# Kernel tuning notes

Measured on AMD Instinct MI355X. Metric: run time of the kernel, lower is better.

## Reference

```python
import jax, jax.numpy as jnp
import numpy as np

KH = KW = 3
K = KH * KW
STRIDE = 1
PAD = 1
DIL = 1
DG = 1  # deformable groups


def conv2d(x, w, b):
    out = jax.lax.conv_general_dilated(
        x, w, window_strides=(STRIDE, STRIDE),
        padding=[(PAD, PAD), (PAD, PAD)], rhs_dilation=(DIL, DIL),
        dimension_numbers=('NCHW', 'OIHW', 'NCHW'))
    return out + b[None, :, None, None]


def deform_conv2d(x, offset, mask, w, b):
    """DCNv2: bilinear sample at predicted offsets, modulate by mask, GEMM with w."""
    B, Cin, H, W = x.shape
    Ho, Wo = offset.shape[2], offset.shape[3]
    cpg = Cin // DG
    # torchvision layout: channel 2*(g*K+k) = dy, 2*(g*K+k)+1 = dx
    off = offset.reshape(B, DG, K, 2, Ho, Wo)
    off_y, off_x = off[:, :, :, 0], off[:, :, :, 1]  # [B,DG,K,Ho,Wo]
    m = mask.reshape(B, DG, K, Ho, Wo)
    ky = jnp.repeat(jnp.arange(KH), KW) * DIL          # [K] kernel row offsets
    kx = jnp.tile(jnp.arange(KW), KH) * DIL            # [K] kernel col offsets
    hh = jnp.arange(Ho) * STRIDE - PAD
    ww = jnp.arange(Wo) * STRIDE - PAD
    py = off_y + ky[None, None, :, None, None] + hh[None, None, None, :, None]
    px = off_x + kx[None, None, :, None, None] + ww[None, None, None, None, :]
    y0 = jnp.floor(py); x0 = jnp.floor(px)
    wy = py - y0; wx = px - x0
    x_g = x.reshape(B, DG, cpg, H * W)

    def gather(yc, xc):  # zero-padded bilinear corner fetch
        valid = ((yc >= 0) & (yc < H) & (xc >= 0) & (xc < W)).astype(x.dtype)
        yi = jnp.clip(yc, 0, H - 1).astype(jnp.int32)
        xi = jnp.clip(xc, 0, W - 1).astype(jnp.int32)
        idx = (yi * W + xi).reshape(B, DG, 1, K * Ho * Wo)
        v = jnp.take_along_axis(x_g, jnp.broadcast_to(idx, (B, DG, cpg, K * Ho * Wo)), axis=3)
        return v.reshape(B, DG, cpg, K, Ho, Wo) * valid[:, :, None]

    v00 = gather(y0, x0)
    v01 = gather(y0, x0 + 1)
    v10 = gather(y0 + 1, x0)
    v11 = gather(y0 + 1, x0 + 1)
    wy_b = wy[:, :, None]; wx_b = wx[:, :, None]  # broadcast over cpg
    sampled = (v00 * (1 - wy_b) * (1 - wx_b) + v01 * (1 - wy_b) * wx_b
               + v10 * wy_b * (1 - wx_b) + v11 * wy_b * wx_b)
    sampled = (sampled * m[:, :, None]).reshape(B, Cin, K, Ho, Wo)
    Cout = w.shape[0]
    out = jnp.einsum('bckhw,ock->bohw', sampled, w.reshape(Cout, Cin, K))
    return out + b[None, :, None, None]


def setup_inputs() -> dict:
    key = jax.random.key(0)
    k1, k2, k3, k4 = jax.random.split(key, 4)
    B, Cin, Cout, H, W = 8, 128, 128, 64, 64
    omc = DG * 3 * K  # 2*K offsets + K mask channels = 27
    x = jax.random.normal(k1, (B, Cin, H, W), dtype=jnp.float32)
    # small offset-conv weights -> modest predicted offsets (mimics near-zero init)
    w_off = jax.random.normal(k2, (omc, Cin, KH, KW), dtype=jnp.float32) * 0.01
    b_off = jnp.zeros((omc,), dtype=jnp.float32)
    w_def = jax.random.normal(k3, (Cout, Cin, KH, KW), dtype=jnp.float32) * (1.0 / np.sqrt(Cin * K))
    b_def = jax.random.normal(k4, (Cout,), dtype=jnp.float32) * 0.01
    return {"x": x, "w_off": w_off, "b_off": b_off, "w_def": w_def, "b_def": b_def}


def reference(x, w_off, b_off, w_def, b_def):
    out = conv2d(x, w_off, b_off)
    oc = DG * 2 * K
    offset = out[:, :oc]
    mask = jax.nn.sigmoid(out[:, oc:])
    return deform_conv2d(x, offset, mask, w_def, b_def)
```

## Files before the change

kernel.cpp:

```cpp
#include <hip/hip_runtime.h>
#include <math.h>

typedef _Float16 f16;
typedef __attribute__((ext_vector_type(2))) _Float16 f16x2;
typedef __attribute__((ext_vector_type(8))) _Float16 f16x8;
typedef __attribute__((ext_vector_type(4))) float f32x4;

#define NBATCH 8
#define WSA_ELE 36864
#define WSB_ELE 147456
#define OFF_WSB  73728
#define OFF_XT   368640
#define OFF_OFFM 8757248

__device__ __forceinline__ void gload_lds16(const f16* gsrc, f16* ldst) {
  __builtin_amdgcn_global_load_lds(
      (const __attribute__((address_space(1))) unsigned int*)gsrc,
      (__attribute__((address_space(3))) unsigned int*)ldst, 16, 0, 0);
}

__global__ __launch_bounds__(256) void prep_w_kernel(const float* __restrict__ w_off,
                                                     const float* __restrict__ w_def,
                                                     f16* __restrict__ wsA,
                                                     f16* __restrict__ wsB) {
  int i = blockIdx.x * 256 + threadIdx.x;
  if (i < WSA_ELE) {
    int j = i & 7, lane = (i >> 3) & 63, fm = i >> 9;
    int ch = fm >> 1, mt = fm & 1;
    int row = mt * 16 + (lane & 15);
    int kidx = ch * 32 + (lane >> 4) * 8 + j;
    int k = kidx >> 7, cc = kidx & 127;
    float v = (row < 27) ? w_off[row * 1152 + cc * 9 + k] : 0.0f;
    wsA[i] = (f16)v;
  } else {
    int e = i - WSA_ELE;
    int j = e & 7, lane = (e >> 3) & 63, fm = e >> 9;
    int ch = fm >> 3, mt = fm & 7;
    int row = mt * 16 + (lane & 15);
    int kidx = ch * 32 + (lane >> 4) * 8 + j;
    int k = kidx >> 7, cc = kidx & 127;
    wsB[e] = (f16)w_def[row * 1152 + cc * 9 + k];
  }
}

__global__ __launch_bounds__(256) void transpose_kernel(const float* __restrict__ x,
                                                        f16* __restrict__ xt) {
  __shared__ f16 s_t[128 * 66];
  const int t = threadIdx.x;
  const int b = blockIdx.x >> 6;
  const int pos0 = (blockIdx.x & 63) << 6;
  const float* xb = x + ((size_t)b << 19);
  for (int i = t; i < 8192; i += 256) {
    int c = i >> 6, p = i & 63;
    s_t[c * 66 + p] = (f16)xb[c * 4096 + pos0 + p];
  }
  __syncthreads();
  f16* xtb = xt + ((size_t)b << 19);
  for (int i = t; i < 4096; i += 256) {
    int p = i >> 6, c2 = (i & 63) * 2;
    unsigned v0 = *(const unsigned short*)&s_t[c2 * 66 + p];
    unsigned v1 = *(const unsigned short*)&s_t[(c2 + 1) * 66 + p];
    *(unsigned*)&xtb[(size_t)(pos0 + p) * 128 + c2] = v0 | (v1 << 16);
  }
}

__global__ __launch_bounds__(256) void offset_conv_kernel(const f16* __restrict__ xt,
                                                          const f16* __restrict__ wsA,
                                                          const float* __restrict__ b_off,
                                                          float* __restrict__ offm) {
  const int t = threadIdx.x;
  const int b = blockIdx.x >> 6, ho = blockIdx.x & 63;
  const int lane = t & 63, wid = t >> 6;
  const int q = lane >> 4, li = lane & 15;
  const int px = (wid << 4) + li;
  const char* xtb = (const char*)xt + ((size_t)b << 20);

  f32x4 acc0 = {0.f, 0.f, 0.f, 0.f}, acc1 = {0.f, 0.f, 0.f, 0.f};

  for (int k = 0; k < 9; ++k) {
    const int ky = k / 3, kx = k - ky * 3;
    const int y = ho + ky - 1;
    const int xx = px + kx - 1;
    const bool valid = ((unsigned)y < 64u) && ((unsigned)xx < 64u);
    const int pos = min(max(y, 0), 63) * 64 + min(max(xx, 0), 63);
    const int voff = pos * 256 + q * 16;
    #pragma unroll
    for (int c4 = 0; c4 < 4; ++c4) {
      union { uint4 u; f16x8 v; } bu;
      bu.u = *(const uint4*)(xtb + voff + c4 * 64);
      if (!valid) { bu.u.x = 0u; bu.u.y = 0u; bu.u.z = 0u; bu.u.w = 0u; }
      const int ch = k * 4 + c4;
      f16x8 a0 = *(const f16x8*)&wsA[(ch * 2    ) * 512 + lane * 8];
      f16x8 a1 = *(const f16x8*)&wsA[(ch * 2 + 1) * 512 + lane * 8];
      acc0 = __builtin_amdgcn_mfma_f32_16x16x32_f16(a0, bu.v, acc0, 0, 0, 0);
      acc1 = __builtin_amdgcn_mfma_f32_16x16x32_f16(a1, bu.v, acc1, 0, 0, 0);
    }
  }

  float* om = offm + (size_t)b * 27 * 4096 + ho * 64 + px;
  #pragma unroll
  for (int mt = 0; mt < 2; ++mt) {
    f32x4 a = mt ? acc1 : acc0;
    #pragma unroll
    for (int r = 0; r < 4; ++r) {
      int oc = mt * 16 + q * 4 + r;
      if (oc < 27) {
        float v = a[r] + b_off[oc];
        if (oc >= 18) v = 1.0f / (1.0f + __expf(-v));
        om[oc * 4096] = v;
      }
    }
  }
}

__global__ __launch_bounds__(256) void dcn_kernel(const f16* __restrict__ xt,
                                                  const f16* __restrict__ wsB,
                                                  const float* __restrict__ offm,
                                                  const float* __restrict__ b_def,
                                                  float* __restrict__ out) {
  __shared__ uint4  s_ofs[576];
  __shared__ float4 s_wt[576];
  __shared__ __align__(16) f16 s_a[2][4096];
  const int t = threadIdx.x;
  const int b = blockIdx.x >> 6, ho = blockIdx.x & 63;
  const int lane = t & 63, wid = t >> 6;
  const int q = lane >> 4, li = lane & 15;
  const int px0 = wid << 4;
  const char* xtb = (const char*)xt + ((size_t)b << 20);

  {
    const int seg = wid * 2;
    gload_lds16(wsB + seg * 512 + lane * 8,       &s_a[0][seg * 512]);
    gload_lds16(wsB + (seg + 1) * 512 + lane * 8, &s_a[0][(seg + 1) * 512]);
  }

  const float* ob = offm + (size_t)b * 27 * 4096 + ho * 64;
  for (int f = t; f < 576; f += 256) {
    int k = f >> 6, p = f & 63;
    int ky = k / 3, kx = k - ky * 3;
    float oy = ob[(2 * k    ) * 4096 + p];
    float ox = ob[(2 * k + 1) * 4096 + p];
    float m  = ob[(18 + k   ) * 4096 + p];
    float py  = oy + (float)(ho + ky - 1);
    float pxf = ox + (float)(p + kx - 1);
    float y0f = floorf(py), x0f = floorf(pxf);
    float wy = py - y0f, wx = pxf - x0f;
    int y0 = (int)y0f, x0 = (int)x0f;
    int y1 = y0 + 1, x1 = x0 + 1;
    bool y0v = (unsigned)y0 < 64u, y1v = (unsigned)y1 < 64u;
    bool x0v = (unsigned)x0 < 64u, x1v = (unsigned)x1 < 64u;
    int y0c = min(max(y0, 0), 63), y1c = min(max(y1, 0), 63);
    int x0c = min(max(x0, 0), 63), x1c = min(max(x1, 0), 63);
    uint4 o4;
    o4.x = (unsigned)((y0c * 64 + x0c) * 256);
    o4.y = (unsigned)((y0c * 64 + x1c) * 256);
    o4.z = (unsigned)((y1c * 64 + x0c) * 256);
    o4.w = (unsigned)((y1c * 64 + x1c) * 256);
    float4 w4;
    w4.x = (y0v && x0v) ? (1.f - wy) * (1.f - wx) * m : 0.f;
    w4.y = (y0v && x1v) ? (1.f - wy) * wx         * m : 0.f;
    w4.z = (y1v && x0v) ? wy         * (1.f - wx) * m : 0.f;
    w4.w = (y1v && x1v) ? wy         * wx         * m : 0.f;
    s_ofs[f] = o4;
    s_wt[f]  = w4;
  }
  __syncthreads();

  f32x4 acc[8];
  #pragma unroll
  for (int mt = 0; mt < 8; ++mt) acc[mt] = (f32x4){0.f, 0.f, 0.f, 0.f};

  for (int k = 0; k < 9; ++k) {
    const int e = k * 64 + px0 + li;
    const uint4  o4 = s_ofs[e];
    const float4 w4 = s_wt[e];
    const unsigned voff0 = o4.x + q * 16, voff1 = o4.y + q * 16;
    const unsigned voff2 = o4.z + q * 16, voff3 = o4.w + q * 16;
    const f16 h0 = (f16)w4.x, h1 = (f16)w4.y, h2 = (f16)w4.z, h3 = (f16)w4.w;
    const f16x2 wp0 = {h0, h0}, wp1 = {h1, h1}, wp2 = {h2, h2}, wp3 = {h3, h3};
    #pragma unroll
    for (int c4 = 0; c4 < 4; ++c4) {
      const int ch = k * 4 + c4;
      if (ch < 35) {
        const int nb = (ch + 1) & 1;
        const int seg = wid * 2;
        const f16* src = wsB + (ch + 1) * 4096;
        gload_lds16(src + seg * 512 + lane * 8,       &s_a[nb][seg * 512]);
        gload_lds16(src + (seg + 1) * 512 + lane * 8, &s_a[nb][(seg + 1) * 512]);
      }
      union { uint4 u; f16x2 h[4]; } d0, d1, d2, d3;
      d0.u = *(const uint4*)(xtb + voff0 + c4 * 64);
      d1.u = *(const uint4*)(xtb + voff1 + c4 * 64);
      d2.u = *(const uint4*)(xtb + voff2 + c4 * 64);
      d3.u = *(const uint4*)(xtb + voff3 + c4 * 64);
      union { f16x2 h[4]; f16x8 v; } bf;
      #pragma unroll
      for (int i = 0; i < 4; ++i) {
        f16x2 s = d0.h[i] * wp0;
        s = s + d1.h[i] * wp1;
        s = s + d2.h[i] * wp2;
        s = s + d3.h[i] * wp3;
        bf.h[i] = s;
      }
      const f16* ab = &s_a[ch & 1][0];
      #pragma unroll
      for (int mt = 0; mt < 8; ++mt) {
        f16x8 a = *(const f16x8*)&ab[(mt * 64 + lane) * 8];
        acc[mt] = __builtin_amdgcn_mfma_f32_16x16x32_f16(a, bf.v, acc[mt], 0, 0, 0);
      }
      __syncthreads();
    }
  }

  float* o = out + (size_t)b * 128 * 4096 + ho * 64 + px0 + li;
  #pragma unroll
  for (int mt = 0; mt < 8; ++mt) {
    #pragma unroll
    for (int r = 0; r < 4; ++r) {
      int oc = mt * 16 + q * 4 + r;
      o[oc * 4096] = acc[mt][r] + b_def[oc];
    }
  }
}

extern "C" void kernel_launch(void* const* d_in, const int* in_sizes, int n_in,
                              void* d_out, int out_size, void* d_ws, size_t ws_size,
                              hipStream_t stream) {
  const float* x     = (const float*)d_in[0];
  const float* w_off = (const float*)d_in[1];
  const float* b_off = (const float*)d_in[2];
  const float* w_def = (const float*)d_in[3];
  const float* b_def = (const float*)d_in[4];
  float* out = (float*)d_out;

  f16*   wsA  = (f16*)d_ws;
  f16*   wsB  = (f16*)((char*)d_ws + OFF_WSB);
  f16*   xt   = (f16*)((char*)d_ws + OFF_XT);
  float* offm = (float*)((char*)d_ws + OFF_OFFM);

  prep_w_kernel<<<dim3((WSA_ELE + WSB_ELE) / 256), dim3(256), 0, stream>>>(w_off, w_def, wsA, wsB);
  transpose_kernel<<<dim3(NBATCH * 64), dim3(256), 0, stream>>>(x, xt);
  offset_conv_kernel<<<dim3(NBATCH * 64), dim3(256), 0, stream>>>(xt, wsA, b_off, offm);
  dcn_kernel<<<dim3(NBATCH * 64), dim3(256), 0, stream>>>(xt, wsB, offm, b_def, out);
}
```

Before: 135.2 us.

## Fuse offset conv into deformable conv kernel and read weights directly from global

Merges the offset/mask convolution kernel into the deformable conv kernel so offsets and masks stay in shared memory, with no round trip through a global workspace buffer and one fewer launch. It also drops the double-buffered LDS staging of the main weight matrix and its per-chunk barriers, loading the fp16 weight fragments straight from global memory (expected to hit in cache) inside the MFMA loop. The trade-off is more global/L2 traffic for weights per block and no explicit prefetch overlap, in exchange for fewer synchronisations and less LDS use.

```diff
diff --git a/kernel.cpp b/kernel.cpp
--- a/kernel.cpp
+++ b/kernel.cpp
@@ -11,13 +11,6 @@
 #define WSB_ELE 147456
 #define OFF_WSB  73728
 #define OFF_XT   368640
-#define OFF_OFFM 8757248
-
-__device__ __forceinline__ void gload_lds16(const f16* gsrc, f16* ldst) {
-  __builtin_amdgcn_global_load_lds(
-      (const __attribute__((address_space(1))) unsigned int*)gsrc,
-      (__attribute__((address_space(3))) unsigned int*)ldst, 16, 0, 0);
-}
 
 __global__ __launch_bounds__(256) void prep_w_kernel(const float* __restrict__ w_off,
                                                      const float* __restrict__ w_def,
@@ -64,10 +57,15 @@
   }
 }
 
-__global__ __launch_bounds__(256) void offset_conv_kernel(const f16* __restrict__ xt,
-                                                          const f16* __restrict__ wsA,
-                                                          const float* __restrict__ b_off,
-                                                          float* __restrict__ offm) {
+__global__ __launch_bounds__(256) void fused_dcn_kernel(const f16* __restrict__ xt,
+                                                        const f16* __restrict__ wsA,
+                                                        const f16* __restrict__ wsB,
+                                                        const float* __restrict__ b_off,
+                                                        const float* __restrict__ b_def,
+                                                        float* __restrict__ out) {
+  __shared__ float  s_off[27 * 65];
+  __shared__ uint4  s_ofs[576];
+  __shared__ float4 s_wt[576];
   const int t = threadIdx.x;
   const int b = blockIdx.x >> 6, ho = blockIdx.x & 63;
   const int lane = t & 63, wid = t >> 6;
@@ -75,72 +73,49 @@
   const int px = (wid << 4) + li;
   const char* xtb = (const char*)xt + ((size_t)b << 20);
 
-  f32x4 acc0 = {0.f, 0.f, 0.f, 0.f}, acc1 = {0.f, 0.f, 0.f, 0.f};
-
-  for (int k = 0; k < 9; ++k) {
-    const int ky = k / 3, kx = k - ky * 3;
-    const int y = ho + ky - 1;
-    const int xx = px + kx - 1;
-    const bool valid = ((unsigned)y < 64u) && ((unsigned)xx < 64u);
-    const int pos = min(max(y, 0), 63) * 64 + min(max(xx, 0), 63);
-    const int voff = pos * 256 + q * 16;
+  {
+    f32x4 acc0 = {0.f, 0.f, 0.f, 0.f}, acc1 = {0.f, 0.f, 0.f, 0.f};
+    for (int k = 0; k < 9; ++k) {
+      const int ky = k / 3, kx = k - ky * 3;
+      const int y = ho + ky - 1;
+      const int xx = px + kx - 1;
+      const bool valid = ((unsigned)y < 64u) && ((unsigned)xx < 64u);
+      const int pos = min(max(y, 0), 63) * 64 + min(max(xx, 0), 63);
+      const int voff = pos * 256 + q * 16;
+      #pragma unroll
+      for (int c4 = 0; c4 < 4; ++c4) {
+        union { uint4 u; f16x8 v; } bu;
+        bu.u = *(const uint4*)(xtb + voff + c4 * 64);
+        if (!valid) { bu.u.x = 0u; bu.u.y = 0u; bu.u.z = 0u; bu.u.w = 0u; }
+        const int ch = k * 4 + c4;
+        f16x8 a0 = *(const f16x8*)&wsA[(ch * 2    ) * 512 + lane * 8];
+        f16x8 a1 = *(const f16x8*)&wsA[(ch * 2 + 1) * 512 + lane * 8];
+        acc0 = __builtin_amdgcn_mfma_f32_16x16x32_f16(a0, bu.v, acc0, 0, 0, 0);
+        acc1 = __builtin_amdgcn_mfma_f32_16x16x32_f16(a1, bu.v, acc1, 0, 0, 0);
+      }
+    }
     #pragma unroll
-    for (int c4 = 0; c4 < 4; ++c4) {
-      union { uint4 u; f16x8 v; } bu;
-      bu.u = *(const uint4*)(xtb + voff + c4 * 64);
-      if (!valid) { bu.u.x = 0u; bu.u.y = 0u; bu.u.z = 0u; bu.u.w = 0u; }
-      const int ch = k * 4 + c4;
-      f16x8 a0 = *(const f16x8*)&wsA[(ch * 2    ) * 512 + lane * 8];
-      f16x8 a1 = *(const f16x8*)&wsA[(ch * 2 + 1) * 512 + lane * 8];
-      acc0 = __builtin_amdgcn_mfma_f32_16x16x32_f16(a0, bu.v, acc0, 0, 0, 0);
-      acc1 = __builtin_amdgcn_mfma_f32_16x16x32_f16(a1, bu.v, acc1, 0, 0, 0);
-    }
-  }
-
-  float* om = offm + (size_t)b * 27 * 4096 + ho * 64 + px;
-  #pragma unroll
-  for (int mt = 0; mt < 2; ++mt) {
-    f32x4 a = mt ? acc1 : acc0;
-    #pragma unroll
-    for (int r = 0; r < 4; ++r) {
-      int oc = mt * 16 + q * 4 + r;
-      if (oc < 27) {
-        float v = a[r] + b_off[oc];
-        if (oc >= 18) v = 1.0f / (1.0f + __expf(-v));
-        om[oc * 4096] = v;
-      }
-    }
-  }
-}
-
-__global__ __launch_bounds__(256) void dcn_kernel(const f16* __restrict__ xt,
-                                                  const f16* __restrict__ wsB,
-                                                  const float* __restrict__ offm,
-                                                  const float* __restrict__ b_def,
-                                                  float* __restrict__ out) {
-  __shared__ uint4  s_ofs[576];
-  __shared__ float4 s_wt[576];
-  __shared__ __align__(16) f16 s_a[2][4096];
-  const int t = threadIdx.x;
-  const int b = blockIdx.x >> 6, ho = blockIdx.x & 63;
-  const int lane = t & 63, wid = t >> 6;
-  const int q = lane >> 4, li = lane & 15;
-  const int px0 = wid << 4;
-  const char* xtb = (const char*)xt + ((size_t)b << 20);
-
-  {
-    const int seg = wid * 2;
-    gload_lds16(wsB + seg * 512 + lane * 8,       &s_a[0][seg * 512]);
-    gload_lds16(wsB + (seg + 1) * 512 + lane * 8, &s_a[0][(seg + 1) * 512]);
-  }
-
-  const float* ob = offm + (size_t)b * 27 * 4096 + ho * 64;
+    for (int mt = 0; mt < 2; ++mt) {
+      f32x4 a = mt ? acc1 : acc0;
+      #pragma unroll
+      for (int r = 0; r < 4; ++r) {
+        int oc = mt * 16 + q * 4 + r;
+        if (oc < 27) {
+          float v = a[r] + b_off[oc];
+          if (oc >= 18) v = 1.0f / (1.0f + __expf(-v));
+          s_off[oc * 65 + px] = v;
+        }
+      }
+    }
+  }
+  __syncthreads();
+
   for (int f = t; f < 576; f += 256) {
     int k = f >> 6, p = f & 63;
     int ky = k / 3, kx = k - ky * 3;
-    float oy = ob[(2 * k    ) * 4096 + p];
-    float ox = ob[(2 * k + 1) * 4096 + p];
-    float m  = ob[(18 + k   ) * 4096 + p];
+    float oy = s_off[(2 * k    ) * 65 + p];
+    float ox = s_off[(2 * k + 1) * 65 + p];
+    float m  = s_off[(18 + k   ) * 65 + p];
     float py  = oy + (float)(ho + ky - 1);
     float pxf = ox + (float)(p + kx - 1);
     float y0f = floorf(py), x0f = floorf(pxf);
@@ -170,8 +145,9 @@
   #pragma unroll
   for (int mt = 0; mt < 8; ++mt) acc[mt] = (f32x4){0.f, 0.f, 0.f, 0.f};
 
+  #pragma unroll 1
   for (int k = 0; k < 9; ++k) {
-    const int e = k * 64 + px0 + li;
+    const int e = k * 64 + px;
     const uint4  o4 = s_ofs[e];
     const float4 w4 = s_wt[e];
     const unsigned voff0 = o4.x + q * 16, voff1 = o4.y + q * 16;
@@ -181,13 +157,6 @@
     #pragma unroll
     for (int c4 = 0; c4 < 4; ++c4) {
       const int ch = k * 4 + c4;
-      if (ch < 35) {
-        const int nb = (ch + 1) & 1;
-        const int seg = wid * 2;
-        const f16* src = wsB + (ch + 1) * 4096;
-        gload_lds16(src + seg * 512 + lane * 8,       &s_a[nb][seg * 512]);
-        gload_lds16(src + (seg + 1) * 512 + lane * 8, &s_a[nb][(seg + 1) * 512]);
-      }
       union { uint4 u; f16x2 h[4]; } d0, d1, d2, d3;
       d0.u = *(const uint4*)(xtb + voff0 + c4 * 64);
       d1.u = *(const uint4*)(xtb + voff1 + c4 * 64);
@@ -202,17 +171,16 @@
         s = s + d3.h[i] * wp3;
         bf.h[i] = s;
       }
-      const f16* ab = &s_a[ch & 1][0];
+      const f16* ab = wsB + (size_t)ch * 4096;
       #pragma unroll
       for (int mt = 0; mt < 8; ++mt) {
         f16x8 a = *(const f16x8*)&ab[(mt * 64 + lane) * 8];
         acc[mt] = __builtin_amdgcn_mfma_f32_16x16x32_f16(a, bf.v, acc[mt], 0, 0, 0);
       }
-      __syncthreads();
-    }
-  }
-
-  float* o = out + (size_t)b * 128 * 4096 + ho * 64 + px0 + li;
+    }
+  }
+
+  float* o = out + (size_t)b * 128 * 4096 + ho * 64 + px;
   #pragma unroll
   for (int mt = 0; mt < 8; ++mt) {
     #pragma unroll
@@ -233,13 +201,11 @@
   const float* b_def = (const float*)d_in[4];
   float* out = (float*)d_out;
 
-  f16*   wsA  = (f16*)d_ws;
-  f16*   wsB  = (f16*)((char*)d_ws + OFF_WSB);
-  f16*   xt   = (f16*)((char*)d_ws + OFF_XT);
-  float* offm = (float*)((char*)d_ws + OFF_OFFM);
+  f16* wsA = (f16*)d_ws;
+  f16* wsB = (f16*)((char*)d_ws + OFF_WSB);
+  f16* xt  = (f16*)((char*)d_ws + OFF_XT);
 
   prep_w_kernel<<<dim3((WSA_ELE + WSB_ELE) / 256), dim3(256), 0, stream>>>(w_off, w_def, wsA, wsB);
   transpose_kernel<<<dim3(NBATCH * 64), dim3(256), 0, stream>>>(x, xt);
-  offset_conv_kernel<<<dim3(NBATCH * 64), dim3(256), 0, stream>>>(xt, wsA, b_off, offm);
-  dcn_kernel<<<dim3(NBATCH * 64), dim3(256), 0, stream>>>(xt, wsB, offm, b_def, out);
-}
+  fused_dcn_kernel<<<dim3(NBATCH * 64), dim3(256), 0, stream>>>(xt, wsA, wsB, b_off, b_def, out);
+}
```

New measurement: 181.5 us. 34.3% more time.
